# Kernel tuning notes

Hardware: AMD Instinct MI355X
Metric: run time of the kernel (lower is better)

Reference implementation:

```python
import jax, jax.numpy as jnp
import numpy as np

N = 2000          # number of proposals
C = 81            # num classes (incl. background)
IMG_H = 800.0
IMG_W = 800.0
SCORE_THRESH = 0.05
NMS_THRESH = 0.5
NUM_DET = 100
MIN_SIZE = 1.0
REG_W = (10.0, 10.0, 5.0, 5.0)
BBOX_CLIP = float(np.log(1000.0 / 16.0))


def setup_inputs() -> dict:
    key = jax.random.key(0)
    k1, k2, k3, k4 = jax.random.split(key, 4)
    class_logit = jax.random.normal(k1, (N, C), jnp.float32) * 2.0
    box_regression = jax.random.normal(k2, (N, C * 4), jnp.float32) * 0.1
    xy = jax.random.uniform(k3, (N, 2), jnp.float32) * (IMG_W - 120.0)
    wh = jax.random.uniform(k4, (N, 2), jnp.float32) * 100.0 + 4.0
    proposal = jnp.concatenate([xy, xy + wh], axis=1)  # valid [x1,y1,x2,y2]
    return {"class_logit": class_logit, "box_regression": box_regression, "proposal": proposal}


def _decode(delta, boxes):
    # BoxCoder.decode with weights REG_W
    w = boxes[:, 2] - boxes[:, 0]
    h = boxes[:, 3] - boxes[:, 1]
    cx = boxes[:, 0] + 0.5 * w
    cy = boxes[:, 1] + 0.5 * h
    dx = delta[:, 0] / REG_W[0]
    dy = delta[:, 1] / REG_W[1]
    dw = jnp.minimum(delta[:, 2] / REG_W[2], BBOX_CLIP)
    dh = jnp.minimum(delta[:, 3] / REG_W[3], BBOX_CLIP)
    pcx = dx * w + cx
    pcy = dy * h + cy
    pw = jnp.exp(dw) * w
    ph = jnp.exp(dh) * h
    return jnp.stack([pcx - 0.5 * pw, pcy - 0.5 * ph, pcx + 0.5 * pw, pcy + 0.5 * ph], axis=1)


def _iou_matrix(b):
    # b: [N,4] -> [N,N]
    area = (b[:, 2] - b[:, 0]) * (b[:, 3] - b[:, 1])
    lt = jnp.maximum(b[:, None, :2], b[None, :, :2])
    rb = jnp.minimum(b[:, None, 2:], b[None, :, 2:])
    whm = jnp.clip(rb - lt, 0.0)
    inter = whm[..., 0] * whm[..., 1]
    return inter / (area[:, None] + area[None, :] - inter + 1e-9)


def _per_class(score, delta, proposal):
    boxes = _decode(delta, proposal)
    boxes = jnp.stack([
        jnp.clip(boxes[:, 0], 0.0, IMG_W),
        jnp.clip(boxes[:, 1], 0.0, IMG_H),
        jnp.clip(boxes[:, 2], 0.0, IMG_W),
        jnp.clip(boxes[:, 3], 0.0, IMG_H),
    ], axis=1)
    bw = boxes[:, 2] - boxes[:, 0]
    bh = boxes[:, 3] - boxes[:, 1]
    valid = (score >= SCORE_THRESH) & (bw >= MIN_SIZE) & (bh >= MIN_SIZE)
    s = jnp.where(valid, score, -1.0)
    order = jnp.argsort(-s)
    bs = boxes[order]
    ss = s[order]
    iou = jax.lax.stop_gradient(_iou_matrix(bs))
    idx = jnp.arange(N)

    def body(i, keep):
        sup = (iou[i] > NMS_THRESH) & (idx > i) & keep[i]
        return keep & (~sup)

    keep = jax.lax.fori_loop(0, N, body, ss >= 0.0)
    final = jnp.where(keep, ss, -1.0)
    topv, topi = jax.lax.top_k(final, NUM_DET)
    return bs[topi], topv, topv >= 0.0


def reference(class_logit, box_regression, proposal):
    pred = jax.nn.softmax(class_logit, axis=-1)               # [N, C]
    deltas = box_regression.reshape(N, C, 4)
    scores_c = pred[:, 1:].T                                   # [C-1, N]
    deltas_c = jnp.transpose(deltas[:, 1:, :], (1, 0, 2))      # [C-1, N, 4]
    boxes, scores, valid = jax.vmap(lambda s, d: _per_class(s, d, proposal))(scores_c, deltas_c)
    labels = jnp.repeat(jnp.arange(1, C, dtype=jnp.int32), NUM_DET)
    return boxes.reshape(-1, 4), scores.reshape(-1), labels, valid.reshape(-1)
```

## Files before the change

### kernel.cpp

```cpp
#include <hip/hip_runtime.h>
#include <math.h>

#define NPROP 2000
#define NCLS  81
#define NFG   80
#define NDET  100
#define NBLK  512
#define VMAX  512
#define WMAX  16

#define PROWS 40
#define PBLK  256

#define IMGW 800.0f
#define IMGH 800.0f
#define SCORE_THRESH 0.05f
#define NMS_THRESH 0.5f
#define MIN_SIZE 1.0f
#define BBOX_CLIP 4.135166556742356f

__global__ __launch_bounds__(PBLK) void prep_kernel(const float* __restrict__ logits,
                                                    const float* __restrict__ reg,
                                                    float* __restrict__ scoreT,
                                                    float* __restrict__ regT) {
    __shared__ float tileL[PROWS * NCLS];
    __shared__ float tileR[PROWS * NCLS * 4];
    __shared__ float s_m[PROWS], s_s[PROWS];
    const int n0 = blockIdx.x * PROWS;

    for (int t = threadIdx.x; t < PROWS * NCLS; t += PBLK)
        tileL[t] = logits[n0 * NCLS + t];
    __syncthreads();

    if (threadIdx.x < PROWS) {
        const float* row = tileL + threadIdx.x * NCLS;
        float m = -1e30f;
        for (int k = 0; k < NCLS; ++k) m = fmaxf(m, row[k]);
        float s = 0.0f;
        for (int k = 0; k < NCLS; ++k) s += expf(row[k] - m);
        s_m[threadIdx.x] = m;
        s_s[threadIdx.x] = s;
    }
    __syncthreads();

    for (int t = threadIdx.x; t < NFG * PROWS; t += PBLK) {
        int cc = t / PROWS, i = t - cc * PROWS;
        float sc = expf(tileL[i * NCLS + (cc + 1)] - s_m[i]) / s_s[i];
        scoreT[cc * NPROP + n0 + i] = sc;
    }

    for (int t = threadIdx.x; t < PROWS * NCLS * 4; t += PBLK)
        tileR[t] = reg[(size_t)n0 * (NCLS * 4) + t];
    __syncthreads();

    for (int t = threadIdx.x; t < NFG * PROWS; t += PBLK) {
        int cc = t / PROWS, i = t - cc * PROWS;
        const float* src = tileR + i * (NCLS * 4) + (cc + 1) * 4;
        float4 v = make_float4(src[0], src[1], src[2], src[3]);
        ((float4*)regT)[cc * NPROP + n0 + i] = v;
    }
}

__global__ __launch_bounds__(NBLK) void perclass_kernel(
        const float* __restrict__ scoreT,
        const float* __restrict__ regT,
        const float* __restrict__ prop,
        float* __restrict__ out) {
    const int cc   = blockIdx.x;
    const int tid  = threadIdx.x;
    const int lane = tid & 63;
    const int wv   = tid >> 6;

    __shared__ float s_x1u[NPROP], s_y1u[NPROP], s_x2u[NPROP], s_y2u[NPROP];
    __shared__ float s_scu[NPROP];
    __shared__ float s_vsc[NPROP];
    __shared__ unsigned short s_vlist[NPROP];
    __shared__ unsigned short s_ord[NPROP];
    __shared__ unsigned char  s_keep[NPROP];
    __shared__ unsigned int   s_supm[VMAX * WMAX];
    __shared__ unsigned short s_keepOut[NDET], s_supOut[NDET], s_invOut[NDET];
    __shared__ int s_cnt, s_K, s_wcnt[8];

    if (tid == 0) s_cnt = 0;
    __syncthreads();

    for (int n = tid; n < NPROP; n += NBLK) {
        float sc = scoreT[cc * NPROP + n];

        float4 pr = ((const float4*)prop)[n];
        float w  = pr.z - pr.x, h = pr.w - pr.y;
        float cx = pr.x + 0.5f * w, cy = pr.y + 0.5f * h;
        float4 d = ((const float4*)regT)[cc * NPROP + n];
        float dx = d.x / 10.0f;
        float dy = d.y / 10.0f;
        float dw = fminf(d.z / 5.0f, BBOX_CLIP);
        float dh = fminf(d.w / 5.0f, BBOX_CLIP);
        float pcx = dx * w + cx;
        float pcy = dy * h + cy;
        float pw  = expf(dw) * w;
        float ph  = expf(dh) * h;
        float bx1 = fminf(fmaxf(pcx - 0.5f * pw, 0.0f), IMGW);
        float by1 = fminf(fmaxf(pcy - 0.5f * ph, 0.0f), IMGH);
        float bx2 = fminf(fmaxf(pcx + 0.5f * pw, 0.0f), IMGW);
        float by2 = fminf(fmaxf(pcy + 0.5f * ph, 0.0f), IMGH);
        s_x1u[n] = bx1; s_y1u[n] = by1; s_x2u[n] = bx2; s_y2u[n] = by2;
        bool valid = (sc >= SCORE_THRESH) && ((bx2 - bx1) >= MIN_SIZE)
                                          && ((by2 - by1) >= MIN_SIZE);
        s_scu[n] = valid ? sc : -1.0f;
        if (valid) {
            int p = atomicAdd(&s_cnt, 1);
            s_vlist[p] = (unsigned short)n;
            s_vsc[p]   = sc;
        }
    }
    __syncthreads();
    const int V = s_cnt;

    for (int i = tid; i < V; i += NBLK) {
        float si = s_vsc[i];
        int   ni = s_vlist[i];
        int r = 0;
        for (int j = 0; j < V; ++j) {
            float sj = s_vsc[j];
            int   nj = s_vlist[j];
            r += (sj > si) || (sj == si && nj < ni);
        }
        s_ord[r] = (unsigned short)ni;
    }
    __syncthreads();

    int K;

    if (V <= VMAX) {
        const int W = (V + 31) >> 5;
        for (int t = tid; t < V * W; t += NBLK) {
            int i = t / W, w = t - i * W;
            int ni = s_ord[i];
            float ax1 = s_x1u[ni], ay1 = s_y1u[ni], ax2 = s_x2u[ni], ay2 = s_y2u[ni];
            float areaA = (ax2 - ax1) * (ay2 - ay1);
            unsigned int bits = 0;
            int jbase = w << 5;
            int jend  = (jbase + 32 < V) ? jbase + 32 : V;
            int j0    = (jbase > i + 1) ? jbase : i + 1;
            for (int j = j0; j < jend; ++j) {
                int nj = s_ord[j];
                float bx1 = s_x1u[nj], by1 = s_y1u[nj], bx2 = s_x2u[nj], by2 = s_y2u[nj];
                float areaB = (bx2 - bx1) * (by2 - by1);
                float lx = fmaxf(ax1, bx1), ly = fmaxf(ay1, by1);
                float rx = fminf(ax2, bx2), ry = fminf(ay2, by2);
                float iw = fmaxf(rx - lx, 0.0f), ih = fmaxf(ry - ly, 0.0f);
                float inter = iw * ih;
                float iou = inter / (areaA + areaB - inter + 1e-9f);
                if (iou > NMS_THRESH) bits |= 1u << (j - jbase);
            }
            s_supm[i * W + w] = bits;
        }
        __syncthreads();

        unsigned int kw = 0;
        if (wv == 0) {
            int base = lane << 5;
            if (base < V) kw = (V - base >= 32) ? 0xffffffffu
                                                : ((1u << (V - base)) - 1u);
            int nk = 0;
            unsigned int nrow = (V > 0 && lane < W) ? s_supm[lane] : 0u;
            for (int i = 0; i < V; ++i) {
                unsigned int rowb = nrow;
                if (i + 1 < V) nrow = (lane < W) ? s_supm[(i + 1) * W + lane] : 0u;
                unsigned int kword = (unsigned int)__shfl((int)kw, i >> 5);
                if ((kword >> (i & 31)) & 1u) {
                    if (lane == 0) s_keepOut[nk] = (unsigned short)i;
                    ++nk;
                    if (nk == NDET) break;
                    kw &= ~rowb;
                }
            }
            if (lane == 0) s_K = nk;
        }
        __syncthreads();
        K = s_K;

        if (K < NDET) {
            if (wv == 0) {
                int b = 0;
                for (int start = 0; start < V && b < NDET; start += 64) {
                    int p = start + lane;
                    unsigned int kword = (unsigned int)__shfl((int)kw, (p >> 5) & 15);
                    bool f = (p < V) && !((kword >> (p & 31)) & 1u);
                    unsigned long long mb = __ballot(f);
                    int pos = b + __popcll(mb & ((1ull << lane) - 1ull));
                    if (f && pos < NDET) s_supOut[pos] = (unsigned short)p;
                    b += (int)__popcll(mb);
                }
            } else if (wv == 1) {
                int b = 0;
                for (int start = 0; start < NPROP && b < NDET; start += 64) {
                    int n = start + lane;
                    bool f = (s_scu[n] < 0.0f);
                    unsigned long long mb = __ballot(f);
                    int pos = b + __popcll(mb & ((1ull << lane) - 1ull));
                    if (f && pos < NDET) s_invOut[pos] = (unsigned short)n;
                    b += (int)__popcll(mb);
                }
            }
        }
        __syncthreads();
    } else {
        for (int p = tid; p < V; p += NBLK) s_keep[p] = 1;
        __syncthreads();
        int nk = 0;
        for (int i = 0; i < V; ++i) {
            if (s_keep[i]) {
                if (tid == 0) s_keepOut[nk] = (unsigned short)i;
                nk++;
                if (nk == NDET) break;
                int ni = s_ord[i];
                float ax1 = s_x1u[ni], ay1 = s_y1u[ni], ax2 = s_x2u[ni], ay2 = s_y2u[ni];
                float areaA = (ax2 - ax1) * (ay2 - ay1);
                for (int j = i + 1 + tid; j < V; j += NBLK) {
                    if (!s_keep[j]) continue;
                    int nj = s_ord[j];
                    float bx1 = s_x1u[nj], by1 = s_y1u[nj], bx2 = s_x2u[nj], by2 = s_y2u[nj];
                    float areaB = (bx2 - bx1) * (by2 - by1);
                    float lx = fmaxf(ax1, bx1), ly = fmaxf(ay1, by1);
                    float rx = fminf(ax2, bx2), ry = fminf(ay2, by2);
                    float iw = fmaxf(rx - lx, 0.0f), ih = fmaxf(ry - ly, 0.0f);
                    float inter = iw * ih;
                    float iou = inter / (areaA + areaB - inter + 1e-9f);
                    if (iou > NMS_THRESH) s_keep[j] = 0;
                }
                __syncthreads();
            }
        }
        if (tid == 0) s_K = nk;
        __syncthreads();
        K = s_K;

        if (K < NDET) {
            int base = 0;
            for (int start = 0; start < V && base < NDET; start += NBLK) {
                int p = start + tid;
                bool f = (p < V) && (!s_keep[p]);
                unsigned long long mb = __ballot(f);
                if (lane == 0) s_wcnt[wv] = __popcll(mb);
                __syncthreads();
                int wbase = base;
                for (int ww = 0; ww < wv; ++ww) wbase += s_wcnt[ww];
                if (f) {
                    int pos = wbase + __popcll(mb & ((1ull << lane) - 1ull));
                    if (pos < NDET) s_supOut[pos] = (unsigned short)p;
                }
                for (int ww = 0; ww < 8; ++ww) base += s_wcnt[ww];
                __syncthreads();
            }
            base = 0;
            for (int start = 0; start < NPROP && base < NDET; start += NBLK) {
                int n = start + tid;
                bool f = (n < NPROP) && (s_scu[n] < 0.0f);
                unsigned long long mb = __ballot(f);
                if (lane == 0) s_wcnt[wv] = __popcll(mb);
                __syncthreads();
                int wbase = base;
                for (int ww = 0; ww < wv; ++ww) wbase += s_wcnt[ww];
                if (f) {
                    int pos = wbase + __popcll(mb & ((1ull << lane) - 1ull));
                    if (pos < NDET) s_invOut[pos] = (unsigned short)n;
                }
                for (int ww = 0; ww < 8; ++ww) base += s_wcnt[ww];
                __syncthreads();
            }
        }
        __syncthreads();
    }

    const int nsupT = (K < NDET) ? (V - K) : 0;

    float* out_boxes  = out;
    float* out_scores = out + NFG * NDET * 4;
    float* out_labels = out + NFG * NDET * 4 + NFG * NDET;
    float* out_valid  = out + NFG * NDET * 4 + 2 * NFG * NDET;
    const int base_o = cc * NDET;

    for (int k = tid; k < NDET; k += NBLK) {
        int n; float sc, vf;
        if (k < K) {
            n = s_ord[s_keepOut[k]];
            sc = s_scu[n]; vf = 1.0f;
        } else {
            int j = k - K;
            n = (j < nsupT) ? s_ord[s_supOut[j]] : s_invOut[j - nsupT];
            sc = -1.0f; vf = 0.0f;
        }
        out_boxes[(base_o + k) * 4 + 0] = s_x1u[n];
        out_boxes[(base_o + k) * 4 + 1] = s_y1u[n];
        out_boxes[(base_o + k) * 4 + 2] = s_x2u[n];
        out_boxes[(base_o + k) * 4 + 3] = s_y2u[n];
        out_scores[base_o + k] = sc;
        out_labels[base_o + k] = (float)(cc + 1);
        out_valid[base_o + k]  = vf;
    }
}

extern "C" void kernel_launch(void* const* d_in, const int* in_sizes, int n_in,
                              void* d_out, int out_size, void* d_ws, size_t ws_size,
                              hipStream_t stream) {
    const float* logits = (const float*)d_in[0];
    const float* reg    = (const float*)d_in[1];
    const float* prop   = (const float*)d_in[2];
    float* out    = (float*)d_out;
    float* scoreT = (float*)d_ws;
    float* regT   = scoreT + NFG * NPROP;

    prep_kernel<<<NPROP / PROWS, PBLK, 0, stream>>>(logits, reg, scoreT, regT);
    perclass_kernel<<<NFG, NBLK, 0, stream>>>(scoreT, regT, prop, out);
}
```

Before: 105.7 us.

## Fuse softmax/transpose prep into per-class NMS kernel via cooperative grid sync

Merges the prep kernel (softmax and transpose of scores and regression deltas) into the per-class NMS kernel. Each of the 80 blocks handles a 25-row slice, then all blocks wait on a cooperative-groups grid sync before per-class processing starts. This removes one kernel launch and its gap, but prep now runs on only 80 blocks instead of 50 smaller ones and adds a grid barrier. The extra shared-memory tiles raise per-block LDS use.

```diff
diff --git a/kernel.cpp b/kernel.cpp
--- a/kernel.cpp
+++ b/kernel.cpp
@@ -1,5 +1,8 @@
 #include <hip/hip_runtime.h>
+#include <hip/hip_cooperative_groups.h>
 #include <math.h>
+
+namespace cg = cooperative_groups;
 
 #define NPROP 2000
 #define NCLS  81
@@ -8,9 +11,7 @@
 #define NBLK  512
 #define VMAX  512
 #define WMAX  16
-
-#define PROWS 40
-#define PBLK  256
+#define SLICE 25
 
 #define IMGW 800.0f
 #define IMGH 800.0f
@@ -19,58 +20,20 @@
 #define MIN_SIZE 1.0f
 #define BBOX_CLIP 4.135166556742356f
 
-__global__ __launch_bounds__(PBLK) void prep_kernel(const float* __restrict__ logits,
-                                                    const float* __restrict__ reg,
-                                                    float* __restrict__ scoreT,
-                                                    float* __restrict__ regT) {
-    __shared__ float tileL[PROWS * NCLS];
-    __shared__ float tileR[PROWS * NCLS * 4];
-    __shared__ float s_m[PROWS], s_s[PROWS];
-    const int n0 = blockIdx.x * PROWS;
-
-    for (int t = threadIdx.x; t < PROWS * NCLS; t += PBLK)
-        tileL[t] = logits[n0 * NCLS + t];
-    __syncthreads();
-
-    if (threadIdx.x < PROWS) {
-        const float* row = tileL + threadIdx.x * NCLS;
-        float m = -1e30f;
-        for (int k = 0; k < NCLS; ++k) m = fmaxf(m, row[k]);
-        float s = 0.0f;
-        for (int k = 0; k < NCLS; ++k) s += expf(row[k] - m);
-        s_m[threadIdx.x] = m;
-        s_s[threadIdx.x] = s;
-    }
-    __syncthreads();
-
-    for (int t = threadIdx.x; t < NFG * PROWS; t += PBLK) {
-        int cc = t / PROWS, i = t - cc * PROWS;
-        float sc = expf(tileL[i * NCLS + (cc + 1)] - s_m[i]) / s_s[i];
-        scoreT[cc * NPROP + n0 + i] = sc;
-    }
-
-    for (int t = threadIdx.x; t < PROWS * NCLS * 4; t += PBLK)
-        tileR[t] = reg[(size_t)n0 * (NCLS * 4) + t];
-    __syncthreads();
-
-    for (int t = threadIdx.x; t < NFG * PROWS; t += PBLK) {
-        int cc = t / PROWS, i = t - cc * PROWS;
-        const float* src = tileR + i * (NCLS * 4) + (cc + 1) * 4;
-        float4 v = make_float4(src[0], src[1], src[2], src[3]);
-        ((float4*)regT)[cc * NPROP + n0 + i] = v;
-    }
-}
-
-__global__ __launch_bounds__(NBLK) void perclass_kernel(
-        const float* __restrict__ scoreT,
-        const float* __restrict__ regT,
+__global__ __launch_bounds__(NBLK) void fused_kernel(
+        const float* __restrict__ logits,
+        const float* __restrict__ reg,
         const float* __restrict__ prop,
+        float* __restrict__ scoreT,
+        float* __restrict__ regT,
         float* __restrict__ out) {
-    const int cc   = blockIdx.x;
     const int tid  = threadIdx.x;
     const int lane = tid & 63;
     const int wv   = tid >> 6;
 
+    __shared__ float tileL[SLICE * NCLS];
+    __shared__ float tileR[SLICE * NCLS * 4];
+    __shared__ float s_m[SLICE], s_s[SLICE];
     __shared__ float s_x1u[NPROP], s_y1u[NPROP], s_x2u[NPROP], s_y2u[NPROP];
     __shared__ float s_scu[NPROP];
     __shared__ float s_vsc[NPROP];
@@ -80,6 +43,41 @@
     __shared__ unsigned int   s_supm[VMAX * WMAX];
     __shared__ unsigned short s_keepOut[NDET], s_supOut[NDET], s_invOut[NDET];
     __shared__ int s_cnt, s_K, s_wcnt[8];
+
+    {
+        const int n0 = blockIdx.x * SLICE;
+        for (int t = tid; t < SLICE * NCLS; t += NBLK)
+            tileL[t] = logits[n0 * NCLS + t];
+        __syncthreads();
+        if (tid < SLICE) {
+            const float* row = tileL + tid * NCLS;
+            float m = -1e30f;
+            for (int k = 0; k < NCLS; ++k) m = fmaxf(m, row[k]);
+            float s = 0.0f;
+            for (int k = 0; k < NCLS; ++k) s += expf(row[k] - m);
+            s_m[tid] = m;
+            s_s[tid] = s;
+        }
+        __syncthreads();
+        for (int t = tid; t < NFG * SLICE; t += NBLK) {
+            int cc = t / SLICE, i = t - cc * SLICE;
+            scoreT[cc * NPROP + n0 + i] =
+                expf(tileL[i * NCLS + (cc + 1)] - s_m[i]) / s_s[i];
+        }
+        for (int t = tid; t < SLICE * NCLS * 4; t += NBLK)
+            tileR[t] = reg[(size_t)n0 * (NCLS * 4) + t];
+        __syncthreads();
+        for (int t = tid; t < NFG * SLICE; t += NBLK) {
+            int cc = t / SLICE, i = t - cc * SLICE;
+            const float* src = tileR + i * (NCLS * 4) + (cc + 1) * 4;
+            ((float4*)regT)[cc * NPROP + n0 + i] =
+                make_float4(src[0], src[1], src[2], src[3]);
+        }
+    }
+    __threadfence();
+    cg::this_grid().sync();
+
+    const int cc = blockIdx.x;
 
     if (tid == 0) s_cnt = 0;
     __syncthreads();
@@ -311,6 +309,8 @@
     float* scoreT = (float*)d_ws;
     float* regT   = scoreT + NFG * NPROP;
 
-    prep_kernel<<<NPROP / PROWS, PBLK, 0, stream>>>(logits, reg, scoreT, regT);
-    perclass_kernel<<<NFG, NBLK, 0, stream>>>(scoreT, regT, prop, out);
+    void* args[] = { (void*)&logits, (void*)&reg, (void*)&prop,
+                     (void*)&scoreT, (void*)&regT, (void*)&out };
+    hipLaunchCooperativeKernel((const void*)fused_kernel,
+                               dim3(NFG), dim3(NBLK), args, 0, stream);
 }
```

Measured after the change: 141.9 us. +34.3%, slower.
